# Performance work log

Hardware: AMD Instinct MI355X
Metric: run time of the kernel (lower is better)

The kernel has to match this reference:

```python
import jax, jax.numpy as jnp
import numpy as np

N, E, H, C = 50000, 800000, 4, 32   # nodes, edges, heads, per-head channels
EMB = 64                              # embedding_dim
VOCAB = 1000                          # input_dim (label vocab)


def _gat_layer(x, src, dst, W, a_src, a_dst, b):
    """PyG GATConv (concat heads, negative_slope=0.2, self-loops already in src/dst)."""
    n = x.shape[0]
    h = (x @ W).reshape(n, H, -1)                 # [N,H,C]
    al_s = (h * a_src).sum(-1)                    # [N,H]
    al_d = (h * a_dst).sum(-1)                    # [N,H]
    e = jax.nn.leaky_relu(al_s[src] + al_d[dst], 0.2)   # [E',H]
    m = jax.ops.segment_max(e, dst, num_segments=n)     # segment softmax (stable)
    p = jnp.exp(e - m[dst])
    s = jax.ops.segment_sum(p, dst, num_segments=n)
    alpha = p / (s[dst] + 1e-16)                  # [E',H]
    out = jax.ops.segment_sum(h[src] * alpha[..., None], dst, num_segments=n)
    return out.reshape(n, -1) + b                 # [N,H*C]


def setup_inputs() -> dict:
    key = jax.random.key(0)
    ks = jax.random.split(key, 16)
    def w(k, shape):
        return jax.random.normal(k, shape, jnp.float32) * 0.1
    return dict(
        label=jax.random.randint(ks[0], (N,), 0, VOCAB),
        edge_index=jax.random.randint(ks[1], (2, E), 0, N),
        weight=jax.random.uniform(ks[2], (E,), jnp.float32),
        request_quantity=jax.random.uniform(ks[3], (N,), jnp.float32),
        emb_table=w(ks[4], (VOCAB, EMB)),
        req_W=w(ks[5], (1, EMB)),
        req_b=jnp.zeros((EMB,), jnp.float32),
        W0=w(ks[6], (2 * EMB, H * C)), a_src0=w(ks[7], (H, C)), a_dst0=w(ks[8], (H, C)), b0=jnp.zeros((H * C,), jnp.float32),
        W1=w(ks[9], (H * C, H * C)), a_src1=w(ks[10], (H, C)), a_dst1=w(ks[11], (H, C)), b1=jnp.zeros((H * C,), jnp.float32),
        W2=w(ks[12], (H * C, H * C)), a_src2=w(ks[13], (H, C)), a_dst2=w(ks[14], (H, C)), b2=jnp.zeros((H * C,), jnp.float32),
    )


def reference(label, edge_index, weight, request_quantity, emb_table, req_W, req_b,
              W0, a_src0, a_dst0, b0, W1, a_src1, a_dst1, b1, W2, a_src2, a_dst2, b2):
    del weight  # GATConv(edge_dim=None): edge weights are not used in attention
    x_emb = emb_table[label]                                  # [N,EMB]
    rq = request_quantity
    rq = (rq - rq.mean()) / (rq.std(ddof=1) + 1e-6)           # torch std uses ddof=1
    req = rq[:, None] @ req_W + req_b                         # [N,EMB]
    x = jnp.concatenate([x_emb, req], axis=-1)                # [N,2*EMB]
    # PyG GATConv adds self-loops by default
    loops = jnp.arange(N)
    src = jnp.concatenate([edge_index[0], loops])
    dst = jnp.concatenate([edge_index[1], loops])
    gelu = lambda t: jax.nn.gelu(t, approximate=False)        # torch nn.GELU is exact
    x = gelu(_gat_layer(x, src, dst, W0, a_src0, a_dst0, b0))
    x = gelu(_gat_layer(x, src, dst, W1, a_src1, a_dst1, b1))
    x = gelu(_gat_layer(x, src, dst, W2, a_src2, a_dst2, b2))
    return x
```

## Files before the change

### kernel.cpp

```cpp
#include <hip/hip_runtime.h>
#include <hip/hip_fp16.h>
#include <math.h>

#define NN 50000
#define NE 800000
#define HC 128
#define EMB 64
#define STATS_BLOCKS 64
#define NB 196
#define HIST_BLOCKS 196
#define WPREP_BLOCKS 192
#define WT_ROW 136
#define GEMM_BLOCKS 782

typedef _Float16 f16x8 __attribute__((ext_vector_type(8)));
typedef float f32x4 __attribute__((ext_vector_type(4)));

__device__ __forceinline__ float lrelu(float x) { return x > 0.0f ? x : 0.2f * x; }
__device__ __forceinline__ float gelu_f(float x) {
    return 0.5f * x * (1.0f + erff(x * 0.70710678118654752440f));
}
__device__ __forceinline__ float sel4(float4 v, int h) {
    float r = v.x;
    r = (h == 1) ? v.y : r;
    r = (h == 2) ? v.z : r;
    r = (h == 3) ? v.w : r;
    return r;
}
__device__ __forceinline__ f16x8 cvt8(float4 a, float4 b) {
    f16x8 v;
    v[0] = (_Float16)a.x; v[1] = (_Float16)a.y; v[2] = (_Float16)a.z; v[3] = (_Float16)a.w;
    v[4] = (_Float16)b.x; v[5] = (_Float16)b.y; v[6] = (_Float16)b.z; v[7] = (_Float16)b.w;
    return v;
}

__global__ void prep_kernel(const float* __restrict__ rq, float* __restrict__ stats,
                            const int* __restrict__ dst, int* __restrict__ bucketCnt,
                            const float* __restrict__ W0, const float* __restrict__ W1,
                            const float* __restrict__ W2, _Float16* __restrict__ wt) {
    __shared__ float ls[4], ls2[4];
    __shared__ int cnt[NB];
    if (blockIdx.x < STATS_BLOCKS) {
        int i = blockIdx.x * 256 + threadIdx.x;
        float s = 0.f, s2 = 0.f;
        for (; i < NN; i += STATS_BLOCKS * 256) {
            float v = rq[i];
            s += v; s2 += v * v;
        }
        #pragma unroll
        for (int off = 32; off > 0; off >>= 1) {
            s  += __shfl_down(s, off);
            s2 += __shfl_down(s2, off);
        }
        int lane = threadIdx.x & 63, wid = threadIdx.x >> 6;
        if (lane == 0) { ls[wid] = s; ls2[wid] = s2; }
        __syncthreads();
        if (threadIdx.x == 0) {
            atomicAdd(&stats[0], ls[0] + ls[1] + ls[2] + ls[3]);
            atomicAdd(&stats[1], ls2[0] + ls2[1] + ls2[2] + ls2[3]);
        }
    } else if (blockIdx.x < STATS_BLOCKS + HIST_BLOCKS) {
        int bb = blockIdx.x - STATS_BLOCKS;
        for (int i = threadIdx.x; i < NB; i += 256) cnt[i] = 0;
        __syncthreads();
        int base = bb * 4096;
        #pragma unroll
        for (int it = 0; it < 16; it++) {
            int i = base + it * 256 + threadIdx.x;
            if (i < NE) atomicAdd(&cnt[dst[i] >> 8], 1);
        }
        __syncthreads();
        for (int i = threadIdx.x; i < NB; i += 256)
            if (cnt[i]) atomicAdd(&bucketCnt[i], cnt[i]);
    } else {
        int bb = blockIdx.x - STATS_BLOCKS - HIST_BLOCKS;
        int l = bb >> 6, blk = bb & 63;
        const float* W = (l == 0) ? W0 : (l == 1) ? W1 : W2;
        int idx = blk * 256 + threadIdx.x;
        int n = idx >> 7, k = idx & 127;
        wt[(size_t)l * 128 * WT_ROW + n * WT_ROW + k] = (_Float16)W[k * 128 + n];
    }
}

__device__ __forceinline__ void scan_buckets(const int* __restrict__ bucketCnt,
                                             int* sIncl ) {
    int t = threadIdx.x;
    int v = (t < NB) ? bucketCnt[t] : 0;
    sIncl[t] = v;
    __syncthreads();
    #pragma unroll
    for (int off = 1; off < 256; off <<= 1) {
        int add = (t >= off) ? sIncl[t - off] : 0;
        __syncthreads();
        sIncl[t] += add;
        __syncthreads();
    }
}

__device__ __forceinline__ void mfma_epilogue(_Float16* sWt, _Float16* sX,
        const float* __restrict__ a_src, const float* __restrict__ a_dst,
        __half* __restrict__ h, float* __restrict__ als, float* __restrict__ ald,
        int row0) {
    int t = threadIdx.x;
    int w = t >> 6, l = t & 63;
    int col = l & 15, quad = l >> 4;

    f16x8 afr[4];
    #pragma unroll
    for (int ks = 0; ks < 4; ks++)
        afr[ks] = *(const f16x8*)&sX[(w * 16 + col) * WT_ROW + ks * 32 + quad * 8];

    f32x4 zero = {0.f, 0.f, 0.f, 0.f};
    f32x4 acc[8];
    #pragma unroll
    for (int nt = 0; nt < 8; nt++) acc[nt] = zero;
    #pragma unroll
    for (int nt = 0; nt < 8; nt++) {
        #pragma unroll
        for (int ks = 0; ks < 4; ks++) {
            f16x8 bfr = *(const f16x8*)&sWt[(nt * 16 + col) * WT_ROW + ks * 32 + quad * 8];
            acc[nt] = __builtin_amdgcn_mfma_f32_16x16x32_f16(afr[ks], bfr, acc[nt], 0, 0, 0);
        }
    }
    __syncthreads();

    _Float16* sOut = sWt;
    #pragma unroll
    for (int nt = 0; nt < 8; nt++)
        #pragma unroll
        for (int r = 0; r < 4; r++)
            sOut[(w * 16 + quad * 4 + r) * WT_ROW + nt * 16 + col] = (_Float16)acc[nt][r];
    __builtin_amdgcn_wave_barrier();
    #pragma unroll
    for (int i = 0; i < 4; i++) {
        int u = l + 64 * i;
        int r = u >> 4, off = (u & 15) * 8;
        int rr = row0 + w * 16 + r;
        f16x8 v = *(const f16x8*)&sOut[(w * 16 + r) * WT_ROW + off];
        if (rr < NN) *(f16x8*)(h + (size_t)rr * 128 + off) = v;
    }

    float as[8], ad[8];
    #pragma unroll
    for (int nt = 0; nt < 8; nt++) {
        as[nt] = a_src[nt * 16 + col];
        ad[nt] = a_dst[nt * 16 + col];
    }
    #pragma unroll
    for (int r = 0; r < 4; r++) {
        float ps[4], pd[4];
        #pragma unroll
        for (int hd = 0; hd < 4; hd++) {
            ps[hd] = acc[2 * hd][r] * as[2 * hd] + acc[2 * hd + 1][r] * as[2 * hd + 1];
            pd[hd] = acc[2 * hd][r] * ad[2 * hd] + acc[2 * hd + 1][r] * ad[2 * hd + 1];
            ps[hd] += __shfl_xor(ps[hd], 1); pd[hd] += __shfl_xor(pd[hd], 1);
            ps[hd] += __shfl_xor(ps[hd], 2); pd[hd] += __shfl_xor(pd[hd], 2);
            ps[hd] += __shfl_xor(ps[hd], 4); pd[hd] += __shfl_xor(pd[hd], 4);
            ps[hd] += __shfl_xor(ps[hd], 8); pd[hd] += __shfl_xor(pd[hd], 8);
        }
        int rr = row0 + w * 16 + quad * 4 + r;
        if (col == 0 && rr < NN) {
            *(float4*)(als + (size_t)rr * 4) = make_float4(ps[0], ps[1], ps[2], ps[3]);
            *(float4*)(ald + (size_t)rr * 4) = make_float4(pd[0], pd[1], pd[2], pd[3]);
        }
    }
}

__launch_bounds__(256)
__global__ void gemm0_binA_kernel(const _Float16* __restrict__ wt,
                                  const float* __restrict__ a_src, const float* __restrict__ a_dst,
                                  __half* __restrict__ h, float* __restrict__ als,
                                  float* __restrict__ ald,
                                  const int* __restrict__ label, const float* __restrict__ rq,
                                  const float* __restrict__ emb, const float* __restrict__ reqW,
                                  const float* __restrict__ reqb, const float* __restrict__ stats,
                                  const int* __restrict__ src, const int* __restrict__ dst,
                                  const int* __restrict__ bucketCnt, int* __restrict__ gcur,
                                  int2* __restrict__ edge_tmp) {
    extern __shared__ char smem[];
    if (blockIdx.x >= GEMM_BLOCKS) {
        int bb = blockIdx.x - GEMM_BLOCKS;
        int* sIncl  = (int*)smem;
        int* sBaseE = sIncl + 256;
        int* cnt    = sBaseE + 256;
        int* cur    = cnt + NB;
        int t = threadIdx.x;
        scan_buckets(bucketCnt, sIncl);
        {
            int v = (t < NB) ? bucketCnt[t] : 0;
            sBaseE[t] = sIncl[t] - v;
        }
        for (int i = t; i < NB; i += 256) cnt[i] = 0;
        __syncthreads();
        int base = bb * 4096;
        int d[16], s[16];
        #pragma unroll
        for (int it = 0; it < 16; it++) {
            int i = base + it * 256 + t;
            bool ok = i < NE;
            d[it] = ok ? dst[i] : -1;
            s[it] = ok ? src[i] : 0;
            if (ok) atomicAdd(&cnt[d[it] >> 8], 1);
        }
        __syncthreads();
        for (int i = t; i < NB; i += 256)
            cur[i] = cnt[i] ? (sBaseE[i] + atomicAdd(&gcur[i], cnt[i])) : 0;
        __syncthreads();
        #pragma unroll
        for (int it = 0; it < 16; it++) {
            if (d[it] >= 0) {
                int b = d[it] >> 8;
                int pos = atomicAdd(&cur[b], 1);
                edge_tmp[pos] = make_int2(s[it], d[it] & 255);
            }
        }
        return;
    }
    _Float16* sWt = (_Float16*)smem;
    _Float16* sX  = sWt + 128 * WT_ROW;
    int t = threadIdx.x;
    int row0 = blockIdx.x * 64;

    {
        const f16x8* g = (const f16x8*)wt;
        f16x8* s = (f16x8*)sWt;
        #pragma unroll
        for (int i = 0; i < 9; i++) {
            int idx = t + 256 * i;
            if (idx < 128 * WT_ROW / 8) s[idx] = g[idx];
        }
    }
    {
        float sum = stats[0], sumsq = stats[1];
        float mean = sum / (float)NN;
        float var = (sumsq - sum * sum / (float)NN) / (float)(NN - 1);
        float inv = 1.0f / (sqrtf(var) + 1e-6f);
        #pragma unroll
        for (int i = 0; i < 4; i++) {
            int idx = t + 256 * i;
            int r = idx >> 4;
            int q = idx & 15;
            int rr = row0 + r;
            f16x8 v;
            #pragma unroll
            for (int j = 0; j < 8; j++) v[j] = (_Float16)0.f;
            if (rr < NN) {
                if (q < 8) {
                    const float4* er = (const float4*)(emb + (size_t)label[rr] * EMB);
                    v = cvt8(er[q * 2], er[q * 2 + 1]);
                } else {
                    int j4 = (q - 8) * 2;
                    float4 w0 = ((const float4*)reqW)[j4],     b0 = ((const float4*)reqb)[j4];
                    float4 w1 = ((const float4*)reqW)[j4 + 1], b1 = ((const float4*)reqb)[j4 + 1];
                    float r2 = (rq[rr] - mean) * inv;
                    v = cvt8(make_float4(r2 * w0.x + b0.x, r2 * w0.y + b0.y,
                                         r2 * w0.z + b0.z, r2 * w0.w + b0.w),
                             make_float4(r2 * w1.x + b1.x, r2 * w1.y + b1.y,
                                         r2 * w1.z + b1.z, r2 * w1.w + b1.w));
                }
            }
            *(f16x8*)&sX[r * WT_ROW + q * 8] = v;
        }
    }
    __syncthreads();
    mfma_epilogue(sWt, sX, a_src, a_dst, h, als, ald, row0);
}

__global__ void binB_kernel(const int2* __restrict__ edge_tmp, const int* __restrict__ bucketCnt,
                            int* __restrict__ row_start, int* __restrict__ src_sorted) {
    __shared__ int sIncl[256];
    __shared__ int ldeg[256];
    __shared__ int lexcl[256];
    __shared__ int lcur[256];
    __shared__ int s_base, s_end;
    int b = blockIdx.x, t = threadIdx.x;
    scan_buckets(bucketCnt, sIncl);
    if (t == 0) {
        s_end = sIncl[b];
        s_base = sIncl[b] - bucketCnt[b];
    }
    ldeg[t] = 0;
    __syncthreads();
    int base = s_base, endb = s_end;
    for (int i = base + t; i < endb; i += 256)
        atomicAdd(&ldeg[edge_tmp[i].y], 1);
    __syncthreads();
    int v = ldeg[t];
    lexcl[t] = v;
    __syncthreads();
    #pragma unroll
    for (int off = 1; off < 256; off <<= 1) {
        int add = (t >= off) ? lexcl[t - off] : 0;
        __syncthreads();
        lexcl[t] += add;
        __syncthreads();
    }
    int excl = lexcl[t] - v;
    int node = b * 256 + t;
    if (node <= NN) row_start[node] = base + excl;
    lcur[t] = excl;
    __syncthreads();
    for (int i = base + t; i < endb; i += 256) {
        int2 e = edge_tmp[i];
        int pos = atomicAdd(&lcur[e.y], 1);
        src_sorted[base + pos] = e.x;
    }
}

__launch_bounds__(64, 3)
__global__ void layer_fused_kernel(const __half* __restrict__ hp, const float* __restrict__ alsp,
                                   const float* __restrict__ aldp, const int* __restrict__ row_start,
                                   const int* __restrict__ src_sorted, const float* __restrict__ biasp,
                                   const _Float16* __restrict__ wt,
                                   const float* __restrict__ a_src, const float* __restrict__ a_dst,
                                   __half* __restrict__ ho, float* __restrict__ also_,
                                   float* __restrict__ aldo) {
    __shared__ _Float16 sX[16 * WT_ROW];
    __shared__ int2 lds_sp[4][130];
    int lane = threadIdx.x;
    int g    = lane >> 4;
    int cg   = lane & 15;
    int c0   = cg * 8;
    int head = cg >> 2;
    int row0 = blockIdx.x * 16;

    for (int round = 0; round < 4; round++) {
        int nb = row0 + round * 4;
        int node = nb + g;

        int rs = row_start[node];
        int re = row_start[node + 1];
        int start = __shfl(rs, 0);
        int end   = __shfl(re, 48);
        int b1 = __shfl(rs, 16), b2 = __shfl(rs, 32), b3 = __shfl(rs, 48);

        float4 adv = *(const float4*)(aldp + (size_t)node * 4);
        float4 avs = *(const float4*)(alsp + (size_t)node * 4);

        float p_self = __expf(lrelu(sel4(avs, head) + sel4(adv, head)));
        float s_sum = p_self;
        float acc[8];
        {
            f16x8 hv = *(const f16x8*)(hp + (size_t)node * 128 + c0);
            #pragma unroll
            for (int j = 0; j < 8; j++) acc[j] = (float)hv[j] * p_self;
        }

        for (int base = start; base < end; base += 128) {
            int j0 = base + lane, j1 = base + 64 + lane;
            bool v0 = j0 < end, v1 = j1 < end;
            int my0 = v0 ? src_sorted[j0] : 0;
            int my1 = v1 ? src_sorted[j1] : 0;
            float4 av0 = *(const float4*)(alsp + (size_t)my0 * 4);
            float4 av1 = *(const float4*)(alsp + (size_t)my1 * 4);
            int o0 = (j0 >= b1) + (j0 >= b2) + (j0 >= b3);
            int o1 = (j1 >= b1) + (j1 >= b2) + (j1 >= b3);
            float4 d0 = *(const float4*)(aldp + (size_t)(nb + (o0 > 3 ? 3 : o0)) * 4);
            float4 d1 = *(const float4*)(aldp + (size_t)(nb + (o1 > 3 ? 3 : o1)) * 4);
            lds_sp[0][lane] = make_int2(my0, __float_as_int(__expf(lrelu(av0.x + d0.x))));
            lds_sp[1][lane] = make_int2(my0, __float_as_int(__expf(lrelu(av0.y + d0.y))));
            lds_sp[2][lane] = make_int2(my0, __float_as_int(__expf(lrelu(av0.z + d0.z))));
            lds_sp[3][lane] = make_int2(my0, __float_as_int(__expf(lrelu(av0.w + d0.w))));
            lds_sp[0][64 + lane] = make_int2(my1, __float_as_int(__expf(lrelu(av1.x + d1.x))));
            lds_sp[1][64 + lane] = make_int2(my1, __float_as_int(__expf(lrelu(av1.y + d1.y))));
            lds_sp[2][64 + lane] = make_int2(my1, __float_as_int(__expf(lrelu(av1.z + d1.z))));
            lds_sp[3][64 + lane] = make_int2(my1, __float_as_int(__expf(lrelu(av1.w + d1.w))));
            __builtin_amdgcn_wave_barrier();

            int lo  = rs > base ? rs : base;
            int hiw = base + 128;
            int hi  = re < hiw ? re : hiw;
            for (int k = lo; k < hi; k += 16) {
                float p[16];
                const __half* ap[16];
                #pragma unroll
                for (int i = 0; i < 16; i++) {
                    int e = k + i;
                    bool val = e < hi;
                    int ec = (val ? e : hi - 1) - base;
                    int2 sp = lds_sp[head][ec];
                    p[i] = val ? __int_as_float(sp.y) : 0.f;
                    ap[i] = hp + (size_t)sp.x * 128 + c0;
                }
                f16x8 raw[16];
                #pragma unroll
                for (int i = 0; i < 16; i++)
                    raw[i] = *(const f16x8*)ap[i];
                #pragma unroll
                for (int i = 0; i < 16; i++) {
                    s_sum += p[i];
                    #pragma unroll
                    for (int jj = 0; jj < 8; jj++)
                        acc[jj] += (float)raw[i][jj] * p[i];
                }
            }
            __builtin_amdgcn_wave_barrier();
        }

        float invs = 1.0f / (s_sum + 1e-16f);
        float4 bv0 = *(const float4*)(biasp + c0);
        float4 bv1 = *(const float4*)(biasp + c0 + 4);
        float ob[8] = {bv0.x, bv0.y, bv0.z, bv0.w, bv1.x, bv1.y, bv1.z, bv1.w};
        f16x8 o;
        #pragma unroll
        for (int jj = 0; jj < 8; jj++)
            o[jj] = (_Float16)gelu_f(acc[jj] * invs + ob[jj]);
        *(f16x8*)&sX[(round * 4 + g) * WT_ROW + c0] = o;
    }
    __builtin_amdgcn_wave_barrier();

    int col = cg, quad = g;
    f16x8 afr[4];
    #pragma unroll
    for (int ks = 0; ks < 4; ks++)
        afr[ks] = *(const f16x8*)&sX[col * WT_ROW + ks * 32 + quad * 8];
    __builtin_amdgcn_wave_barrier();

    f32x4 zero = {0.f, 0.f, 0.f, 0.f};
    f32x4 acc2[8];
    #pragma unroll
    for (int nt = 0; nt < 8; nt++) acc2[nt] = zero;
    #pragma unroll
    for (int nt = 0; nt < 8; nt++) {
        #pragma unroll
        for (int ks = 0; ks < 4; ks++) {
            f16x8 bfr = *(const f16x8*)&wt[(nt * 16 + col) * WT_ROW + ks * 32 + quad * 8];
            acc2[nt] = __builtin_amdgcn_mfma_f32_16x16x32_f16(afr[ks], bfr, acc2[nt], 0, 0, 0);
        }
    }

    _Float16* sOut = sX;
    #pragma unroll
    for (int nt = 0; nt < 8; nt++)
        #pragma unroll
        for (int r = 0; r < 4; r++)
            sOut[(quad * 4 + r) * WT_ROW + nt * 16 + col] = (_Float16)acc2[nt][r];
    __builtin_amdgcn_wave_barrier();
    #pragma unroll
    for (int i = 0; i < 4; i++) {
        int u = lane + 64 * i;
        int r = u >> 4, off2 = (u & 15) * 8;
        int rr = row0 + r;
        f16x8 v = *(const f16x8*)&sOut[r * WT_ROW + off2];
        if (rr < NN) *(f16x8*)(ho + (size_t)rr * 128 + off2) = v;
    }

    float as[8], ad[8];
    #pragma unroll
    for (int nt = 0; nt < 8; nt++) {
        as[nt] = a_src[nt * 16 + col];
        ad[nt] = a_dst[nt * 16 + col];
    }
    #pragma unroll
    for (int r = 0; r < 4; r++) {
        float ps[4], pd[4];
        #pragma unroll
        for (int hd = 0; hd < 4; hd++) {
            ps[hd] = acc2[2 * hd][r] * as[2 * hd] + acc2[2 * hd + 1][r] * as[2 * hd + 1];
            pd[hd] = acc2[2 * hd][r] * ad[2 * hd] + acc2[2 * hd + 1][r] * ad[2 * hd + 1];
            ps[hd] += __shfl_xor(ps[hd], 1); pd[hd] += __shfl_xor(pd[hd], 1);
            ps[hd] += __shfl_xor(ps[hd], 2); pd[hd] += __shfl_xor(pd[hd], 2);
            ps[hd] += __shfl_xor(ps[hd], 4); pd[hd] += __shfl_xor(pd[hd], 4);
            ps[hd] += __shfl_xor(ps[hd], 8); pd[hd] += __shfl_xor(pd[hd], 8);
        }
        int rr = row0 + quad * 4 + r;
        if (col == 0 && rr < NN) {
            *(float4*)(also_ + (size_t)rr * 4) = make_float4(ps[0], ps[1], ps[2], ps[3]);
            *(float4*)(aldo + (size_t)rr * 4) = make_float4(pd[0], pd[1], pd[2], pd[3]);
        }
    }
}

__launch_bounds__(256)
__global__ void agg_final_kernel(const __half* __restrict__ h, const float* __restrict__ als_,
                                 const float* __restrict__ ald_, const int* __restrict__ row_start,
                                 const int* __restrict__ src_sorted, const float* __restrict__ bias,
                                 float* __restrict__ outf) {
    __shared__ int2 lds_sp[4][4][130];
    int wid  = threadIdx.x >> 6;
    int lane = threadIdx.x & 63;
    int g    = lane >> 4;
    int cg   = lane & 15;
    int c0   = cg * 8;
    int head = cg >> 2;

    int nb = blockIdx.x * 16 + wid * 4;
    if (nb >= NN) return;
    int node = nb + g;

    int rs = row_start[node];
    int re = row_start[node + 1];
    int start = __shfl(rs, 0);
    int end   = __shfl(re, 48);
    int b1 = __shfl(rs, 16), b2 = __shfl(rs, 32), b3 = __shfl(rs, 48);

    float4 adv = *(const float4*)(ald_ + (size_t)node * 4);
    float4 avs = *(const float4*)(als_ + (size_t)node * 4);

    float p_self = __expf(lrelu(sel4(avs, head) + sel4(adv, head)));
    float s_sum = p_self;
    float acc[8];
    {
        f16x8 hv = *(const f16x8*)(h + (size_t)node * 128 + c0);
        #pragma unroll
        for (int j = 0; j < 8; j++) acc[j] = (float)hv[j] * p_self;
    }

    for (int base = start; base < end; base += 128) {
        int j0 = base + lane, j1 = base + 64 + lane;
        bool v0 = j0 < end, v1 = j1 < end;
        int my0 = v0 ? src_sorted[j0] : 0;
        int my1 = v1 ? src_sorted[j1] : 0;
        float4 av0 = *(const float4*)(als_ + (size_t)my0 * 4);
        float4 av1 = *(const float4*)(als_ + (size_t)my1 * 4);
        int o0 = (j0 >= b1) + (j0 >= b2) + (j0 >= b3);
        int o1 = (j1 >= b1) + (j1 >= b2) + (j1 >= b3);
        float4 d0 = *(const float4*)(ald_ + (size_t)(nb + (o0 > 3 ? 3 : o0)) * 4);
        float4 d1 = *(const float4*)(ald_ + (size_t)(nb + (o1 > 3 ? 3 : o1)) * 4);
        lds_sp[wid][0][lane] = make_int2(my0, __float_as_int(__expf(lrelu(av0.x + d0.x))));
        lds_sp[wid][1][lane] = make_int2(my0, __float_as_int(__expf(lrelu(av0.y + d0.y))));
        lds_sp[wid][2][lane] = make_int2(my0, __float_as_int(__expf(lrelu(av0.z + d0.z))));
        lds_sp[wid][3][lane] = make_int2(my0, __float_as_int(__expf(lrelu(av0.w + d0.w))));
        lds_sp[wid][0][64 + lane] = make_int2(my1, __float_as_int(__expf(lrelu(av1.x + d1.x))));
        lds_sp[wid][1][64 + lane] = make_int2(my1, __float_as_int(__expf(lrelu(av1.y + d1.y))));
        lds_sp[wid][2][64 + lane] = make_int2(my1, __float_as_int(__expf(lrelu(av1.z + d1.z))));
        lds_sp[wid][3][64 + lane] = make_int2(my1, __float_as_int(__expf(lrelu(av1.w + d1.w))));
        __builtin_amdgcn_wave_barrier();

        int lo  = rs > base ? rs : base;
        int hiw = base + 128;
        int hi  = re < hiw ? re : hiw;
        for (int k = lo; k < hi; k += 16) {
            float p[16];
            const __half* ap[16];
            #pragma unroll
            for (int i = 0; i < 16; i++) {
                int e = k + i;
                bool val = e < hi;
                int ec = (val ? e : hi - 1) - base;
                int2 sp = lds_sp[wid][head][ec];
                p[i] = val ? __int_as_float(sp.y) : 0.f;
                ap[i] = h + (size_t)sp.x * 128 + c0;
            }
            f16x8 raw[16];
            #pragma unroll
            for (int i = 0; i < 16; i++)
                raw[i] = *(const f16x8*)ap[i];
            #pragma unroll
            for (int i = 0; i < 16; i++) {
                s_sum += p[i];
                #pragma unroll
                for (int jj = 0; jj < 8; jj++)
                    acc[jj] += (float)raw[i][jj] * p[i];
            }
        }
        __builtin_amdgcn_wave_barrier();
    }

    float invs = 1.0f / (s_sum + 1e-16f);
    float4 bv0 = *(const float4*)(bias + c0);
    float4 bv1 = *(const float4*)(bias + c0 + 4);
    float ob[8] = {bv0.x, bv0.y, bv0.z, bv0.w, bv1.x, bv1.y, bv1.z, bv1.w};
    float o8[8];
    #pragma unroll
    for (int jj = 0; jj < 8; jj++) o8[jj] = gelu_f(acc[jj] * invs + ob[jj]);
    float* op = outf + (size_t)node * 128 + c0;
    *(float4*)op       = make_float4(o8[0], o8[1], o8[2], o8[3]);
    *(float4*)(op + 4) = make_float4(o8[4], o8[5], o8[6], o8[7]);
}

extern "C" void kernel_launch(void* const* d_in, const int* in_sizes, int n_in,
                              void* d_out, int out_size, void* d_ws, size_t ws_size,
                              hipStream_t stream) {
    const int*   label = (const int*)d_in[0];
    const int*   eidx  = (const int*)d_in[1];
    const float* rq    = (const float*)d_in[3];
    const float* emb   = (const float*)d_in[4];
    const float* reqW  = (const float*)d_in[5];
    const float* reqb  = (const float*)d_in[6];
    const float* W[3]    = {(const float*)d_in[7],  (const float*)d_in[11], (const float*)d_in[15]};
    const float* asrc[3] = {(const float*)d_in[8],  (const float*)d_in[12], (const float*)d_in[16]};
    const float* adst[3] = {(const float*)d_in[9],  (const float*)d_in[13], (const float*)d_in[17]};
    const float* bias[3] = {(const float*)d_in[10], (const float*)d_in[14], (const float*)d_in[18]};

    const int* e_src = eidx;
    const int* e_dst = eidx + NE;

    char* ws = (char*)d_ws;
    size_t off = 0;
    auto A = [&](size_t n) { size_t o = off; off += (n + 255) & ~(size_t)255; return o; };
    size_t o_bcnt  = A(256 * 4);
    size_t o_gcur  = A(256 * 4);
    size_t o_stats = A(8);
    size_t zero_bytes = off;
    size_t o_row   = A((size_t)(NN + 1) * 4);
    size_t o_etmp  = A((size_t)NE * 8);
    size_t o_srcS  = A((size_t)NE * 4);
    size_t o_wt    = A((size_t)3 * 128 * WT_ROW * 2);
    size_t o_h0    = A((size_t)NN * 128 * 2);
    size_t o_h1    = A((size_t)NN * 128 * 2);
    size_t o_als0  = A((size_t)NN * 4 * 4);
    size_t o_ald0  = A((size_t)NN * 4 * 4);
    size_t o_als1  = A((size_t)NN * 4 * 4);
    size_t o_ald1  = A((size_t)NN * 4 * 4);
    (void)ws_size; (void)n_in; (void)in_sizes; (void)out_size;

    int*      bcnt  = (int*)(ws + o_bcnt);
    int*      gcur  = (int*)(ws + o_gcur);
    float*    stats = (float*)(ws + o_stats);
    int*      rowst = (int*)(ws + o_row);
    int2*     etmp  = (int2*)(ws + o_etmp);
    int*      srcS  = (int*)(ws + o_srcS);
    _Float16* wt    = (_Float16*)(ws + o_wt);
    __half*   h0    = (__half*)(ws + o_h0);
    __half*   h1    = (__half*)(ws + o_h1);
    float*    als0  = (float*)(ws + o_als0);
    float*    ald0  = (float*)(ws + o_ald0);
    float*    als1  = (float*)(ws + o_als1);
    float*    ald1  = (float*)(ws + o_ald1);

    (void)hipMemsetAsync(ws, 0, zero_bytes, stream);

    const int smem_l0 = (128 + 64) * WT_ROW * 2;

    prep_kernel<<<STATS_BLOCKS + HIST_BLOCKS + WPREP_BLOCKS, 256, 0, stream>>>(
        rq, stats, e_dst, bcnt, W[0], W[1], W[2], wt);
    gemm0_binA_kernel<<<GEMM_BLOCKS + HIST_BLOCKS, 256, smem_l0, stream>>>(
        wt, asrc[0], adst[0], h0, als0, ald0, label, rq, emb, reqW, reqb, stats,
        e_src, e_dst, bcnt, gcur, etmp);
    binB_kernel<<<NB, 256, 0, stream>>>(etmp, bcnt, rowst, srcS);
    layer_fused_kernel<<<(NN + 15) / 16, 64, 0, stream>>>(
        h0, als0, ald0, rowst, srcS, bias[0],
        wt + (size_t)1 * 128 * WT_ROW, asrc[1], adst[1], h1, als1, ald1);
    layer_fused_kernel<<<(NN + 15) / 16, 64, 0, stream>>>(
        h1, als1, ald1, rowst, srcS, bias[1],
        wt + (size_t)2 * 128 * WT_ROW, asrc[2], adst[2], h0, als0, ald0);
    agg_final_kernel<<<(NN + 15) / 16, 256, 0, stream>>>(
        h0, als0, ald0, rowst, srcS, bias[2], (float*)d_out);
}
```

Measured before the change: 283.4 us.

## Prefetch edge scores for all four node rounds before aggregation

Splits the per-round loop into two phases. The first loads row bounds, self-loop weights and the first 128-edge chunk of attention scores for all four 4-node groups into a larger LDS buffer. The second phase then does the feature gathers, so the latency of the index and score loads overlaps across rounds instead of being serialized. The gather now uses 32-bit byte offsets instead of 64-bit pointers to cut address arithmetic. In exchange, LDS use per block rises fourfold and more values stay live in registers, which could lower occupancy.

```diff
diff --git a/kernel.cpp b/kernel.cpp
--- a/kernel.cpp
+++ b/kernel.cpp
@@ -316,7 +316,7 @@
                                    __half* __restrict__ ho, float* __restrict__ also_,
                                    float* __restrict__ aldo) {
     __shared__ _Float16 sX[16 * WT_ROW];
-    __shared__ int2 lds_sp[4][130];
+    __shared__ int2 lds_sp[4][4][130];
     int lane = threadIdx.x;
     int g    = lane >> 4;
     int cg   = lane & 15;
@@ -324,30 +324,27 @@
     int head = cg >> 2;
     int row0 = blockIdx.x * 16;
 
-    for (int round = 0; round < 4; round++) {
-        int nb = row0 + round * 4;
+    int rsA[4], reA[4], stA[4], enA[4];
+    float pselfA[4];
+
+    #pragma unroll
+    for (int r = 0; r < 4; r++) {
+        int nb = row0 + r * 4;
         int node = nb + g;
-
         int rs = row_start[node];
         int re = row_start[node + 1];
+        rsA[r] = rs; reA[r] = re;
         int start = __shfl(rs, 0);
         int end   = __shfl(re, 48);
+        stA[r] = start; enA[r] = end;
         int b1 = __shfl(rs, 16), b2 = __shfl(rs, 32), b3 = __shfl(rs, 48);
 
         float4 adv = *(const float4*)(aldp + (size_t)node * 4);
         float4 avs = *(const float4*)(alsp + (size_t)node * 4);
-
-        float p_self = __expf(lrelu(sel4(avs, head) + sel4(adv, head)));
-        float s_sum = p_self;
-        float acc[8];
-        {
-            f16x8 hv = *(const f16x8*)(hp + (size_t)node * 128 + c0);
-            #pragma unroll
-            for (int j = 0; j < 8; j++) acc[j] = (float)hv[j] * p_self;
-        }
-
-        for (int base = start; base < end; base += 128) {
-            int j0 = base + lane, j1 = base + 64 + lane;
+        pselfA[r] = __expf(lrelu(sel4(avs, head) + sel4(adv, head)));
+
+        if (start < end) {
+            int j0 = start + lane, j1 = start + 64 + lane;
             bool v0 = j0 < end, v1 = j1 < end;
             int my0 = v0 ? src_sorted[j0] : 0;
             int my1 = v1 ? src_sorted[j1] : 0;
@@ -357,35 +354,76 @@
             int o1 = (j1 >= b1) + (j1 >= b2) + (j1 >= b3);
             float4 d0 = *(const float4*)(aldp + (size_t)(nb + (o0 > 3 ? 3 : o0)) * 4);
             float4 d1 = *(const float4*)(aldp + (size_t)(nb + (o1 > 3 ? 3 : o1)) * 4);
-            lds_sp[0][lane] = make_int2(my0, __float_as_int(__expf(lrelu(av0.x + d0.x))));
-            lds_sp[1][lane] = make_int2(my0, __float_as_int(__expf(lrelu(av0.y + d0.y))));
-            lds_sp[2][lane] = make_int2(my0, __float_as_int(__expf(lrelu(av0.z + d0.z))));
-            lds_sp[3][lane] = make_int2(my0, __float_as_int(__expf(lrelu(av0.w + d0.w))));
-            lds_sp[0][64 + lane] = make_int2(my1, __float_as_int(__expf(lrelu(av1.x + d1.x))));
-            lds_sp[1][64 + lane] = make_int2(my1, __float_as_int(__expf(lrelu(av1.y + d1.y))));
-            lds_sp[2][64 + lane] = make_int2(my1, __float_as_int(__expf(lrelu(av1.z + d1.z))));
-            lds_sp[3][64 + lane] = make_int2(my1, __float_as_int(__expf(lrelu(av1.w + d1.w))));
-            __builtin_amdgcn_wave_barrier();
+            lds_sp[r][0][lane] = make_int2(my0, __float_as_int(__expf(lrelu(av0.x + d0.x))));
+            lds_sp[r][1][lane] = make_int2(my0, __float_as_int(__expf(lrelu(av0.y + d0.y))));
+            lds_sp[r][2][lane] = make_int2(my0, __float_as_int(__expf(lrelu(av0.z + d0.z))));
+            lds_sp[r][3][lane] = make_int2(my0, __float_as_int(__expf(lrelu(av0.w + d0.w))));
+            lds_sp[r][0][64 + lane] = make_int2(my1, __float_as_int(__expf(lrelu(av1.x + d1.x))));
+            lds_sp[r][1][64 + lane] = make_int2(my1, __float_as_int(__expf(lrelu(av1.y + d1.y))));
+            lds_sp[r][2][64 + lane] = make_int2(my1, __float_as_int(__expf(lrelu(av1.z + d1.z))));
+            lds_sp[r][3][64 + lane] = make_int2(my1, __float_as_int(__expf(lrelu(av1.w + d1.w))));
+        }
+    }
+    __builtin_amdgcn_wave_barrier();
+
+    #pragma unroll
+    for (int r = 0; r < 4; r++) {
+        int nb = row0 + r * 4;
+        int node = nb + g;
+        int rs = rsA[r], re = reA[r];
+        float s_sum = pselfA[r];
+        float acc[8];
+        {
+            f16x8 hv = *(const f16x8*)((const char*)hp + (size_t)node * 256 + c0 * 2);
+            #pragma unroll
+            for (int j = 0; j < 8; j++) acc[j] = (float)hv[j] * pselfA[r];
+        }
+
+        for (int base = stA[r]; base < enA[r]; base += 128) {
+            if (base != stA[r]) {
+                int b1 = __shfl(rs, 16), b2 = __shfl(rs, 32), b3 = __shfl(rs, 48);
+                int end = enA[r];
+                int j0 = base + lane, j1 = base + 64 + lane;
+                bool v0 = j0 < end, v1 = j1 < end;
+                int my0 = v0 ? src_sorted[j0] : 0;
+                int my1 = v1 ? src_sorted[j1] : 0;
+                float4 av0 = *(const float4*)(alsp + (size_t)my0 * 4);
+                float4 av1 = *(const float4*)(alsp + (size_t)my1 * 4);
+                int o0 = (j0 >= b1) + (j0 >= b2) + (j0 >= b3);
+                int o1 = (j1 >= b1) + (j1 >= b2) + (j1 >= b3);
+                float4 d0 = *(const float4*)(aldp + (size_t)(nb + (o0 > 3 ? 3 : o0)) * 4);
+                float4 d1 = *(const float4*)(aldp + (size_t)(nb + (o1 > 3 ? 3 : o1)) * 4);
+                __builtin_amdgcn_wave_barrier();
+                lds_sp[r][0][lane] = make_int2(my0, __float_as_int(__expf(lrelu(av0.x + d0.x))));
+                lds_sp[r][1][lane] = make_int2(my0, __float_as_int(__expf(lrelu(av0.y + d0.y))));
+                lds_sp[r][2][lane] = make_int2(my0, __float_as_int(__expf(lrelu(av0.z + d0.z))));
+                lds_sp[r][3][lane] = make_int2(my0, __float_as_int(__expf(lrelu(av0.w + d0.w))));
+                lds_sp[r][0][64 + lane] = make_int2(my1, __float_as_int(__expf(lrelu(av1.x + d1.x))));
+                lds_sp[r][1][64 + lane] = make_int2(my1, __float_as_int(__expf(lrelu(av1.y + d1.y))));
+                lds_sp[r][2][64 + lane] = make_int2(my1, __float_as_int(__expf(lrelu(av1.z + d1.z))));
+                lds_sp[r][3][64 + lane] = make_int2(my1, __float_as_int(__expf(lrelu(av1.w + d1.w))));
+                __builtin_amdgcn_wave_barrier();
+            }
 
             int lo  = rs > base ? rs : base;
             int hiw = base + 128;
             int hi  = re < hiw ? re : hiw;
             for (int k = lo; k < hi; k += 16) {
                 float p[16];
-                const __half* ap[16];
+                int off[16];
                 #pragma unroll
                 for (int i = 0; i < 16; i++) {
                     int e = k + i;
                     bool val = e < hi;
                     int ec = (val ? e : hi - 1) - base;
-                    int2 sp = lds_sp[head][ec];
+                    int2 sp = lds_sp[r][head][ec];
                     p[i] = val ? __int_as_float(sp.y) : 0.f;
-                    ap[i] = hp + (size_t)sp.x * 128 + c0;
+                    off[i] = sp.x * 256 + c0 * 2;
                 }
                 f16x8 raw[16];
                 #pragma unroll
                 for (int i = 0; i < 16; i++)
-                    raw[i] = *(const f16x8*)ap[i];
+                    raw[i] = *(const f16x8*)((const char*)hp + off[i]);
                 #pragma unroll
                 for (int i = 0; i < 16; i++) {
                     s_sum += p[i];
@@ -394,7 +432,6 @@
                         acc[jj] += (float)raw[i][jj] * p[i];
                 }
             }
-            __builtin_amdgcn_wave_barrier();
         }
 
         float invs = 1.0f / (s_sum + 1e-16f);
@@ -405,7 +442,7 @@
         #pragma unroll
         for (int jj = 0; jj < 8; jj++)
             o[jj] = (_Float16)gelu_f(acc[jj] * invs + ob[jj]);
-        *(f16x8*)&sX[(round * 4 + g) * WT_ROW + c0] = o;
+        *(f16x8*)&sX[(r * 4 + g) * WT_ROW + c0] = o;
     }
     __builtin_amdgcn_wave_barrier();
 
```

Measured after the change: 293.7 us. 1.04x slower.
